# Performance work log

Hardware: AMD Instinct MI355X
Metric: run time of the kernel (lower is better)

## Reference

```python
import jax, jax.numpy as jnp
import numpy as np

B, IN_E, IN_I, D = 4096, 4096, 4096, 2048
IN_BR = 8192
BS = IN_BR // D  # block size = 4
K_E, K_I = 50, 1
E_TO_I = 50.0
BN_EPS = 1e-5


def setup_inputs() -> dict:
    key = jax.random.key(0)
    ks = jax.random.split(key, 8)
    # fan-in uniform init like nn.Linear (kaiming-uniform bound ~ 1/sqrt(in))
    def linw(k, out_f, in_f):
        b = 1.0 / np.sqrt(in_f)
        return jax.random.uniform(k, (out_f, in_f), jnp.float32, -b, b)
    return {
        "excitatory_input": jax.random.normal(ks[0], (B, IN_E), jnp.float32),
        "inhibitory_input": jax.random.normal(ks[1], (B, IN_I), jnp.float32),
        "dendrite_branch_outputs": jax.random.uniform(ks[2], (B, IN_BR), jnp.float32),
        "w_exc": linw(ks[3], D, IN_E),
        "w_inh": linw(ks[4], D, IN_I),
        "w_block": linw(ks[5], D, IN_BR),
        "bn_gamma": jnp.ones((D,), jnp.float32),
        "bn_beta": jnp.zeros((D,), jnp.float32),
    }


def _topk_linear(x, w, k):
    # keep the k largest weights per output row, zero the rest, then matmul
    idx = jax.lax.top_k(w, k)[1]                          # [D, k]
    mask = jnp.zeros_like(w).at[jnp.arange(w.shape[0])[:, None], idx].set(1.0)
    return x @ (w * mask).T                               # [B, D]


def _block_linear(x, w):
    # block-diagonal mask: row c uses columns [c*BS, (c+1)*BS)
    out_f = w.shape[0]
    wb = w.reshape(out_f, out_f, BS)[jnp.arange(out_f), jnp.arange(out_f)]  # [D, BS]
    xb = x.reshape(x.shape[0], out_f, BS)                                   # [B, D, BS]
    return jnp.einsum('bds,ds->bd', xb, wb)


def reference(excitatory_input, inhibitory_input, dendrite_branch_outputs,
              w_exc, w_inh, w_block, bn_gamma, bn_beta):
    dendrite_excitation = _topk_linear(excitatory_input, w_exc, K_E)
    dendrite_inhibition = _topk_linear(inhibitory_input, w_inh, K_I)
    dendrite_depolarization = _block_linear(dendrite_branch_outputs, w_block)
    total_excitatory = dendrite_excitation + dendrite_depolarization
    # neuron_type == 'excitatory'
    act = total_excitatory - E_TO_I * dendrite_inhibition
    # BatchNorm1d, training mode: batch stats, biased variance
    mean = jnp.mean(act, axis=0)
    var = jnp.var(act, axis=0)
    act = (act - mean) * jax.lax.rsqrt(var + BN_EPS) * bn_gamma + bn_beta
    return jax.nn.sigmoid(act)
```

## Files before the change

### kernel.cpp

```cpp
#include <hip/hip_runtime.h>
#include <hip/hip_fp16.h>

#define B_     4096
#define INE_   4096
#define INBR_  8192
#define D_     2048
#define KE_    50
#define KPAD_  52
#define CAP_   512

__device__ __forceinline__ unsigned packh2(float a, float b) {
  __half2 h = __floats2half2_rn(a, b);
  return __builtin_bit_cast(unsigned, h);
}
__device__ __forceinline__ float2 unpackh2(unsigned u) {
  __half2 h = __builtin_bit_cast(__half2, u);
  return __half22float2(h);
}

__global__ __launch_bounds__(256) void extract_diag(
    const float* __restrict__ wblock, float* __restrict__ wdiag)
{
  int d = blockIdx.x * 256 + threadIdx.x;
  float4 w = *reinterpret_cast<const float4*>(wblock + (size_t)d * (INBR_ + 4));
  reinterpret_cast<float4*>(wdiag)[d] = w;
}

__global__ __launch_bounds__(256) void topk_kernel(
    const float* __restrict__ W, int k, int kpad, float hi, float t0,
    float vscale, unsigned* __restrict__ out_off, float* __restrict__ out_val)
{
  const int row = blockIdx.x;
  const int t   = threadIdx.x;
  const float* wr = W + (size_t)row * INE_;

  __shared__ float cval[CAP_];
  __shared__ int   ccol[CAP_];
  __shared__ int   scnt;
  __shared__ int   red[4];

  float thr = t0;
  int M = 0;
  for (int attempt = 0; attempt < 8; ++attempt) {
    int local = 0;
    #pragma unroll
    for (int j = 0; j < 4; ++j) {
      float4 w4 = *reinterpret_cast<const float4*>(wr + 4 * (t + 256 * j));
      local += (w4.x > thr) + (w4.y > thr) + (w4.z > thr) + (w4.w > thr);
    }
    #pragma unroll
    for (int off = 32; off > 0; off >>= 1) local += __shfl_down(local, off);
    if ((t & 63) == 0) red[t >> 6] = local;
    __syncthreads();
    M = red[0] + red[1] + red[2] + red[3];
    __syncthreads();
    if (M >= k && M <= CAP_) break;
    if (M < k) thr = hi - (hi - thr) * 4.0f;
    else       thr = hi - (hi - thr) * 0.5f;
  }

  if (t == 0) scnt = 0;
  __syncthreads();
  #pragma unroll
  for (int j = 0; j < 4; ++j) {
    int cbase = 4 * (t + 256 * j);
    float4 w4 = *reinterpret_cast<const float4*>(wr + cbase);
    float wv[4] = {w4.x, w4.y, w4.z, w4.w};
    #pragma unroll
    for (int q = 0; q < 4; ++q) {
      if (wv[q] > thr) {
        int p = atomicAdd(&scnt, 1);
        if (p < CAP_) { cval[p] = wv[q]; ccol[p] = cbase + q; }
      }
    }
  }
  __syncthreads();
  M = scnt < CAP_ ? scnt : CAP_;

  for (int i = t; i < M; i += 256) {
    float wi = cval[i]; int ci = ccol[i];
    int rank = 0;
    for (int m = 0; m < M; ++m) {
      float wm = cval[m]; int cm = ccol[m];
      rank += (wm > wi || (wm == wi && cm < ci)) ? 1 : 0;
    }
    if (rank < k) {
      unsigned c = (unsigned)ci;
      unsigned off = ((c >> 2) << 4) | ((c & 3u) << 14);
      float    val = wi * vscale;
      if (kpad == 1) {
        out_off[row] = off;
        out_val[row] = val;
      } else {
        size_t idx = ((size_t)(rank >> 2) * D_ + row) * 4 + (rank & 3);
        out_off[idx] = off;
        out_val[idx] = val;
      }
    }
  }
  if (kpad > 1 && t < kpad - k) {
    int slot = k + t;
    size_t idx = ((size_t)(slot >> 2) * D_ + row) * 4 + (slot & 3);
    out_off[idx] = 0u;
    out_val[idx] = 0.0f;
  }
}

__device__ __forceinline__ void stage_rows(const float* __restrict__ src,
                                           unsigned* xs, int b0, int p, int Q) {
  const float* r0p = src + (size_t)(b0 + 2 * p)     * INE_;
  const float* r1p = src + (size_t)(b0 + 2 * p + 1) * INE_;
  #pragma unroll
  for (int m = 0; m < 8; ++m) {
    int c0 = 4 * Q + 512 * m;
    float4 fa = *reinterpret_cast<const float4*>(r0p + c0);
    float4 fb = *reinterpret_cast<const float4*>(r1p + c0);
    int wb = 4 * (Q + 128 * m) + p;
    xs[wb]          = packh2(fa.x, fb.x);
    xs[wb + 4096]   = packh2(fa.y, fb.y);
    xs[wb + 8192]   = packh2(fa.z, fb.z);
    xs[wb + 12288]  = packh2(fa.w, fb.w);
  }
}

#define GATH(R, OFF, WV) do {                                              \
    uint4 xq = *reinterpret_cast<const uint4*>(ldsb + (OFF));              \
    float2 f0 = unpackh2(xq.x), f1 = unpackh2(xq.y);                       \
    float2 f2 = unpackh2(xq.z), f3 = unpackh2(xq.w);                       \
    acc[R][0] = fmaf(f0.x, (WV), acc[R][0]);                               \
    acc[R][1] = fmaf(f0.y, (WV), acc[R][1]);                               \
    acc[R][2] = fmaf(f1.x, (WV), acc[R][2]);                               \
    acc[R][3] = fmaf(f1.y, (WV), acc[R][3]);                               \
    acc[R][4] = fmaf(f2.x, (WV), acc[R][4]);                               \
    acc[R][5] = fmaf(f2.y, (WV), acc[R][5]);                               \
    acc[R][6] = fmaf(f3.x, (WV), acc[R][6]);                               \
    acc[R][7] = fmaf(f3.y, (WV), acc[R][7]);                               \
  } while (0)

__global__ __launch_bounds__(512, 4) void fused_main(
    const float* __restrict__ xe, const float* __restrict__ xi,
    const float* __restrict__ xbr, const float* __restrict__ wdiag,
    const unsigned* __restrict__ soT, const float* __restrict__ veT,
    const unsigned* __restrict__ so_inh, const float* __restrict__ vi_inh,
    float* __restrict__ act)
{
  __shared__ unsigned xs[16384];
  const int t  = threadIdx.x;
  const int b0 = blockIdx.x * 8;
  const int p  = t & 3;
  const int Q  = t >> 2;

  float acc[4][8];
  #pragma unroll
  for (int r = 0; r < 4; ++r)
    #pragma unroll
    for (int b = 0; b < 8; ++b) acc[r][b] = 0.0f;

  const char* ldsb = reinterpret_cast<const char*>(xs);
  const uint4*  soT4 = reinterpret_cast<const uint4*>(soT);
  const float4* veT4 = reinterpret_cast<const float4*>(veT);

  stage_rows(xe, xs, b0, p, Q);
  __syncthreads();
  for (int ii = 0; ii < KPAD_ / 4; ++ii) {
    uint4 o[4]; float4 v[4];
    #pragma unroll
    for (int r = 0; r < 4; ++r) {
      const int d = t + 512 * r;
      o[r] = soT4[ii * D_ + d];
      v[r] = veT4[ii * D_ + d];
    }
    #pragma unroll
    for (int r = 0; r < 4; ++r) {
      GATH(r, o[r].x, v[r].x);
      GATH(r, o[r].y, v[r].y);
      GATH(r, o[r].z, v[r].z);
      GATH(r, o[r].w, v[r].w);
    }
  }
  __syncthreads();

  stage_rows(xi, xs, b0, p, Q);
  unsigned oi[4]; float vi[4];
  #pragma unroll
  for (int r = 0; r < 4; ++r) {
    const int d = t + 512 * r;
    oi[r] = so_inh[d];
    vi[r] = vi_inh[d];
  }
  __syncthreads();
  #pragma unroll
  for (int r = 0; r < 4; ++r) GATH(r, oi[r], vi[r]);

  #pragma unroll
  for (int r = 0; r < 4; ++r) {
    const int d = t + 512 * r;
    float4 wb4 = reinterpret_cast<const float4*>(wdiag)[d];
    #pragma unroll
    for (int b = 0; b < 8; ++b) {
      float4 xb4 = *reinterpret_cast<const float4*>(
          xbr + (size_t)(b0 + b) * INBR_ + 4 * d);
      acc[r][b] += xb4.x * wb4.x + xb4.y * wb4.y + xb4.z * wb4.z + xb4.w * wb4.w;
    }
  }

  #pragma unroll
  for (int r = 0; r < 4; ++r) {
    const int d = t + 512 * r;
    #pragma unroll
    for (int b = 0; b < 8; ++b)
      act[(size_t)(b0 + b) * D_ + d] = acc[r][b];
  }
}

__global__ __launch_bounds__(256) void reduce_stats(
    const float* __restrict__ act, float* __restrict__ sums,
    float* __restrict__ sumsq)
{
  const int dg = blockIdx.x & 63;
  const int rg = blockIdx.x >> 6;
  const int tx = threadIdx.x & 31;
  const int ty = threadIdx.x >> 5;
  const int d  = dg * 32 + tx;

  float s = 0.0f, s2 = 0.0f;
  #pragma unroll 4
  for (int i = 0; i < 64; ++i) {
    int row = rg * 512 + ty + 8 * i;
    float a = act[(size_t)row * D_ + d];
    s += a;
    s2 = fmaf(a, a, s2);
  }
  __shared__ float ls[2][8][32];
  ls[0][ty][tx] = s;
  ls[1][ty][tx] = s2;
  __syncthreads();
  if (ty == 0) {
    #pragma unroll
    for (int j = 1; j < 8; ++j) { s += ls[0][j][tx]; s2 += ls[1][j][tx]; }
    atomicAdd(&sums[d], s);
    atomicAdd(&sumsq[d], s2);
  }
}

__global__ __launch_bounds__(256) void finalize_stats(
    const float* __restrict__ sums, const float* __restrict__ sumsq,
    const float* __restrict__ gamma, const float* __restrict__ beta,
    float* __restrict__ scsh)
{
  int d = blockIdx.x * 256 + threadIdx.x;
  if (d < D_) {
    float mean = sums[d]  * (1.0f / B_);
    float var  = sumsq[d] * (1.0f / B_) - mean * mean;
    float rstd = rsqrtf(var + 1e-5f);
    float sc   = gamma[d] * rstd;
    scsh[2 * d]     = sc;
    scsh[2 * d + 1] = fmaf(-mean, sc, beta[d]);
  }
}

__global__ __launch_bounds__(256) void norm_sigmoid(
    float* __restrict__ act, const float* __restrict__ scsh)
{
  const int total4 = (B_ * D_) / 4;
  for (int i = blockIdx.x * blockDim.x + threadIdx.x; i < total4;
       i += gridDim.x * blockDim.x) {
    float4 a = reinterpret_cast<float4*>(act)[i];
    int d0 = (i * 4) & (D_ - 1);
    const float4* sp = reinterpret_cast<const float4*>(scsh + 2 * d0);
    float4 s0 = sp[0];
    float4 s1 = sp[1];
    float z0 = fmaf(a.x, s0.x, s0.y);
    float z1 = fmaf(a.y, s0.z, s0.w);
    float z2 = fmaf(a.z, s1.x, s1.y);
    float z3 = fmaf(a.w, s1.z, s1.w);
    a.x = 1.0f / (1.0f + __expf(-z0));
    a.y = 1.0f / (1.0f + __expf(-z1));
    a.z = 1.0f / (1.0f + __expf(-z2));
    a.w = 1.0f / (1.0f + __expf(-z3));
    reinterpret_cast<float4*>(act)[i] = a;
  }
}

extern "C" void kernel_launch(void* const* d_in, const int* in_sizes, int n_in,
                              void* d_out, int out_size, void* d_ws, size_t ws_size,
                              hipStream_t stream) {
  const float* xe    = (const float*)d_in[0];
  const float* xi    = (const float*)d_in[1];
  const float* xbr   = (const float*)d_in[2];
  const float* wexc  = (const float*)d_in[3];
  const float* winh  = (const float*)d_in[4];
  const float* wblk  = (const float*)d_in[5];
  const float* gamma = (const float*)d_in[6];
  const float* beta  = (const float*)d_in[7];
  float* act = (float*)d_out;

  char* ws = (char*)d_ws;
  unsigned* soT    = (unsigned*)(ws + 0);
  float*    veT    = (float*)   (ws + 425984);
  unsigned* so_inh = (unsigned*)(ws + 851968);
  float*    vi_inh = (float*)   (ws + 860160);
  float*    wdiag  = (float*)   (ws + 868352);
  float*    sums   = (float*)   (ws + 901120);
  float*    sumsq  = (float*)   (ws + 909312);
  float*    scsh   = (float*)   (ws + 917504);

  hipMemsetAsync(sums, 0, 2 * D_ * sizeof(float), stream);

  const float hi = 0.015625f;
  extract_diag<<<dim3(8), dim3(256), 0, stream>>>(wblk, wdiag);
  topk_kernel<<<dim3(D_), dim3(256), 0, stream>>>(
      wexc, KE_, KPAD_, hi, hi * (1.0f - 200.0f / 4096.0f), 1.0f, soT, veT);
  topk_kernel<<<dim3(D_), dim3(256), 0, stream>>>(
      winh, 1, 1, hi, hi * (1.0f - 48.0f / 4096.0f), -50.0f, so_inh, vi_inh);
  fused_main<<<dim3(B_ / 8), dim3(512), 0, stream>>>(
      xe, xi, xbr, wdiag, soT, veT, so_inh, vi_inh, act);
  reduce_stats<<<dim3(512), dim3(256), 0, stream>>>(act, sums, sumsq);
  finalize_stats<<<dim3((D_ + 255) / 256), dim3(256), 0, stream>>>(
      sums, sumsq, gamma, beta, scsh);
  norm_sigmoid<<<dim3(2048), dim3(256), 0, stream>>>(act, scsh);
}
```

Baseline: 140.0 us.

## Merge prep kernels, split branch term out of main, fuse BN finalize into sigmoid

The top-k selections for both weight matrices and the diagonal extraction now run in a single prep launch. The block-diagonal branch term moves out of the gather kernel into a separate elementwise kernel that reads and rewrites act. The gather loop is restructured to issue LDS loads in batches before the FMAs. The finalize step is folded into the norm/sigmoid kernel, with each block recomputing scale and shift into shared memory. The aim is fewer launches and better latency hiding in the gather, at the cost of an extra full read-modify-write pass over act and redundant per-block statistics computation.

```diff
diff --git a/kernel.cpp b/kernel.cpp
--- a/kernel.cpp
+++ b/kernel.cpp
@@ -18,20 +18,11 @@
   return __half22float2(h);
 }
 
-__global__ __launch_bounds__(256) void extract_diag(
-    const float* __restrict__ wblock, float* __restrict__ wdiag)
-{
-  int d = blockIdx.x * 256 + threadIdx.x;
-  float4 w = *reinterpret_cast<const float4*>(wblock + (size_t)d * (INBR_ + 4));
-  reinterpret_cast<float4*>(wdiag)[d] = w;
-}
-
-__global__ __launch_bounds__(256) void topk_kernel(
-    const float* __restrict__ W, int k, int kpad, float hi, float t0,
-    float vscale, unsigned* __restrict__ out_off, float* __restrict__ out_val)
-{
-  const int row = blockIdx.x;
-  const int t   = threadIdx.x;
+__device__ void topk_body(const float* __restrict__ W, int row, int k, int kpad,
+                          float hi, float t0, float vscale,
+                          unsigned* __restrict__ out_off, float* __restrict__ out_val)
+{
+  const int t = threadIdx.x;
   const float* wr = W + (size_t)row * INE_;
 
   __shared__ float cval[CAP_];
@@ -69,8 +60,8 @@
     #pragma unroll
     for (int q = 0; q < 4; ++q) {
       if (wv[q] > thr) {
-        int p = atomicAdd(&scnt, 1);
-        if (p < CAP_) { cval[p] = wv[q]; ccol[p] = cbase + q; }
+        int pp = atomicAdd(&scnt, 1);
+        if (pp < CAP_) { cval[pp] = wv[q]; ccol[pp] = cbase + q; }
       }
     }
   }
@@ -106,8 +97,34 @@
   }
 }
 
-__device__ __forceinline__ void stage_rows(const float* __restrict__ src,
-                                           unsigned* xs, int b0, int p, int Q) {
+__global__ __launch_bounds__(256) void prep_kernel(
+    const float* __restrict__ wexc, const float* __restrict__ winh,
+    const float* __restrict__ wblk,
+    unsigned* __restrict__ soT, float* __restrict__ veT,
+    unsigned* __restrict__ so_inh, float* __restrict__ vi_inh,
+    float* __restrict__ wdiag)
+{
+  const int bid = blockIdx.x;
+  const float hi = 0.015625f;
+  if (bid < 2048) {
+    topk_body(wexc, bid, KE_, KPAD_, hi, hi * (1.0f - 200.0f / 4096.0f), 1.0f,
+              soT, veT);
+  } else if (bid < 4096) {
+    topk_body(winh, bid - 2048, 1, 1, hi, hi * (1.0f - 48.0f / 4096.0f), -50.0f,
+              so_inh, vi_inh);
+  } else {
+    const int t = threadIdx.x;
+    #pragma unroll
+    for (int j = 0; j < 8; ++j) {
+      int d = t + 256 * j;
+      float4 w = *reinterpret_cast<const float4*>(wblk + (size_t)d * (INBR_ + 4));
+      reinterpret_cast<float4*>(wdiag)[d] = w;
+    }
+  }
+}
+
+__device__ __forceinline__ void stage_rows8(const float* __restrict__ src,
+                                            unsigned* xs, int b0, int p, int Q) {
   const float* r0p = src + (size_t)(b0 + 2 * p)     * INE_;
   const float* r1p = src + (size_t)(b0 + 2 * p + 1) * INE_;
   #pragma unroll
@@ -123,10 +140,13 @@
   }
 }
 
-#define GATH(R, OFF, WV) do {                                              \
-    uint4 xq = *reinterpret_cast<const uint4*>(ldsb + (OFF));              \
-    float2 f0 = unpackh2(xq.x), f1 = unpackh2(xq.y);                       \
-    float2 f2 = unpackh2(xq.z), f3 = unpackh2(xq.w);                       \
+__device__ __forceinline__ uint4 ld16(const char* ldsb, unsigned off) {
+  return *reinterpret_cast<const uint4*>(ldsb + off);
+}
+
+#define FMA8(R, G, WV) do {                                                \
+    float2 f0 = unpackh2((G).x), f1 = unpackh2((G).y);                     \
+    float2 f2 = unpackh2((G).z), f3 = unpackh2((G).w);                     \
     acc[R][0] = fmaf(f0.x, (WV), acc[R][0]);                               \
     acc[R][1] = fmaf(f0.y, (WV), acc[R][1]);                               \
     acc[R][2] = fmaf(f1.x, (WV), acc[R][2]);                               \
@@ -137,9 +157,8 @@
     acc[R][7] = fmaf(f3.y, (WV), acc[R][7]);                               \
   } while (0)
 
-__global__ __launch_bounds__(512, 4) void fused_main(
+__global__ __launch_bounds__(512, 4) void ei_kernel(
     const float* __restrict__ xe, const float* __restrict__ xi,
-    const float* __restrict__ xbr, const float* __restrict__ wdiag,
     const unsigned* __restrict__ soT, const float* __restrict__ veT,
     const unsigned* __restrict__ so_inh, const float* __restrict__ vi_inh,
     float* __restrict__ act)
@@ -160,56 +179,99 @@
   const uint4*  soT4 = reinterpret_cast<const uint4*>(soT);
   const float4* veT4 = reinterpret_cast<const float4*>(veT);
 
-  stage_rows(xe, xs, b0, p, Q);
+  stage_rows8(xe, xs, b0, p, Q);
   __syncthreads();
   for (int ii = 0; ii < KPAD_ / 4; ++ii) {
     uint4 o[4]; float4 v[4];
     #pragma unroll
     for (int r = 0; r < 4; ++r) {
-      const int d = t + 512 * r;
-      o[r] = soT4[ii * D_ + d];
-      v[r] = veT4[ii * D_ + d];
-    }
-    #pragma unroll
-    for (int r = 0; r < 4; ++r) {
-      GATH(r, o[r].x, v[r].x);
-      GATH(r, o[r].y, v[r].y);
-      GATH(r, o[r].z, v[r].z);
-      GATH(r, o[r].w, v[r].w);
-    }
-  }
-  __syncthreads();
-
-  stage_rows(xi, xs, b0, p, Q);
-  unsigned oi[4]; float vi[4];
+      o[r] = soT4[ii * D_ + t + 512 * r];
+      v[r] = veT4[ii * D_ + t + 512 * r];
+    }
+    {
+      uint4 g[2][4];
+      #pragma unroll
+      for (int rr = 0; rr < 2; ++rr) {
+        g[rr][0] = ld16(ldsb, o[rr].x);
+        g[rr][1] = ld16(ldsb, o[rr].y);
+        g[rr][2] = ld16(ldsb, o[rr].z);
+        g[rr][3] = ld16(ldsb, o[rr].w);
+      }
+      #pragma unroll
+      for (int rr = 0; rr < 2; ++rr) {
+        FMA8(rr, g[rr][0], v[rr].x);
+        FMA8(rr, g[rr][1], v[rr].y);
+        FMA8(rr, g[rr][2], v[rr].z);
+        FMA8(rr, g[rr][3], v[rr].w);
+      }
+    }
+    {
+      uint4 g[2][4];
+      #pragma unroll
+      for (int rr = 0; rr < 2; ++rr) {
+        g[rr][0] = ld16(ldsb, o[2 + rr].x);
+        g[rr][1] = ld16(ldsb, o[2 + rr].y);
+        g[rr][2] = ld16(ldsb, o[2 + rr].z);
+        g[rr][3] = ld16(ldsb, o[2 + rr].w);
+      }
+      #pragma unroll
+      for (int rr = 0; rr < 2; ++rr) {
+        FMA8(2 + rr, g[rr][0], v[2 + rr].x);
+        FMA8(2 + rr, g[rr][1], v[2 + rr].y);
+        FMA8(2 + rr, g[rr][2], v[2 + rr].z);
+        FMA8(2 + rr, g[rr][3], v[2 + rr].w);
+      }
+    }
+  }
+  __syncthreads();
+
+  stage_rows8(xi, xs, b0, p, Q);
+  unsigned oi[4]; float viv[4];
+  #pragma unroll
+  for (int r = 0; r < 4; ++r) {
+    oi[r]  = so_inh[t + 512 * r];
+    viv[r] = vi_inh[t + 512 * r];
+  }
+  __syncthreads();
+  {
+    uint4 gi[4];
+    #pragma unroll
+    for (int r = 0; r < 4; ++r) gi[r] = ld16(ldsb, oi[r]);
+    #pragma unroll
+    for (int r = 0; r < 4; ++r) FMA8(r, gi[r], viv[r]);
+  }
+
   #pragma unroll
   for (int r = 0; r < 4; ++r) {
     const int d = t + 512 * r;
-    oi[r] = so_inh[d];
-    vi[r] = vi_inh[d];
-  }
-  __syncthreads();
-  #pragma unroll
-  for (int r = 0; r < 4; ++r) GATH(r, oi[r], vi[r]);
-
-  #pragma unroll
-  for (int r = 0; r < 4; ++r) {
-    const int d = t + 512 * r;
-    float4 wb4 = reinterpret_cast<const float4*>(wdiag)[d];
-    #pragma unroll
-    for (int b = 0; b < 8; ++b) {
-      float4 xb4 = *reinterpret_cast<const float4*>(
-          xbr + (size_t)(b0 + b) * INBR_ + 4 * d);
-      acc[r][b] += xb4.x * wb4.x + xb4.y * wb4.y + xb4.z * wb4.z + xb4.w * wb4.w;
-    }
-  }
-
-  #pragma unroll
-  for (int r = 0; r < 4; ++r) {
-    const int d = t + 512 * r;
     #pragma unroll
     for (int b = 0; b < 8; ++b)
       act[(size_t)(b0 + b) * D_ + d] = acc[r][b];
+  }
+}
+
+__global__ __launch_bounds__(256) void br_kernel(
+    const float* __restrict__ xbr, const float* __restrict__ wdiag,
+    float* __restrict__ act)
+{
+  const float4* xbr4 = reinterpret_cast<const float4*>(xbr);
+  const float4* wd4  = reinterpret_cast<const float4*>(wdiag);
+  float4*       act4 = reinterpret_cast<float4*>(act);
+  const int total = B_ * D_ / 4;
+  for (int i = blockIdx.x * 256 + threadIdx.x; i < total;
+       i += gridDim.x * 256) {
+    int b  = i >> 9;
+    int dq = i & 511;
+    float4 a = act4[i];
+    const float4* xp = xbr4 + (size_t)b * (INBR_ / 4) + 4 * dq;
+    float4 x0 = xp[0], x1 = xp[1], x2 = xp[2], x3 = xp[3];
+    float4 w0 = wd4[4 * dq], w1 = wd4[4 * dq + 1],
+           w2 = wd4[4 * dq + 2], w3 = wd4[4 * dq + 3];
+    a.x += x0.x * w0.x + x0.y * w0.y + x0.z * w0.z + x0.w * w0.w;
+    a.y += x1.x * w1.x + x1.y * w1.y + x1.z * w1.z + x1.w * w1.w;
+    a.z += x2.x * w2.x + x2.y * w2.y + x2.z * w2.z + x2.w * w2.w;
+    a.w += x3.x * w3.x + x3.y * w3.y + x3.z * w3.z + x3.w * w3.w;
+    act4[i] = a;
   }
 }
 
@@ -243,13 +305,16 @@
   }
 }
 
-__global__ __launch_bounds__(256) void finalize_stats(
-    const float* __restrict__ sums, const float* __restrict__ sumsq,
-    const float* __restrict__ gamma, const float* __restrict__ beta,
-    float* __restrict__ scsh)
-{
-  int d = blockIdx.x * 256 + threadIdx.x;
-  if (d < D_) {
+__global__ __launch_bounds__(256) void tail_kernel(
+    float* __restrict__ act, const float* __restrict__ sums,
+    const float* __restrict__ sumsq, const float* __restrict__ gamma,
+    const float* __restrict__ beta)
+{
+  __shared__ float scsh[2 * D_];
+  const int tid = threadIdx.x;
+  #pragma unroll
+  for (int j = 0; j < 8; ++j) {
+    int d = tid + 256 * j;
     float mean = sums[d]  * (1.0f / B_);
     float var  = sumsq[d] * (1.0f / B_) - mean * mean;
     float rstd = rsqrtf(var + 1e-5f);
@@ -257,28 +322,28 @@
     scsh[2 * d]     = sc;
     scsh[2 * d + 1] = fmaf(-mean, sc, beta[d]);
   }
-}
-
-__global__ __launch_bounds__(256) void norm_sigmoid(
-    float* __restrict__ act, const float* __restrict__ scsh)
-{
-  const int total4 = (B_ * D_) / 4;
-  for (int i = blockIdx.x * blockDim.x + threadIdx.x; i < total4;
-       i += gridDim.x * blockDim.x) {
-    float4 a = reinterpret_cast<float4*>(act)[i];
-    int d0 = (i * 4) & (D_ - 1);
-    const float4* sp = reinterpret_cast<const float4*>(scsh + 2 * d0);
-    float4 s0 = sp[0];
-    float4 s1 = sp[1];
-    float z0 = fmaf(a.x, s0.x, s0.y);
-    float z1 = fmaf(a.y, s0.z, s0.w);
-    float z2 = fmaf(a.z, s1.x, s1.y);
-    float z3 = fmaf(a.w, s1.z, s1.w);
-    a.x = 1.0f / (1.0f + __expf(-z0));
-    a.y = 1.0f / (1.0f + __expf(-z1));
-    a.z = 1.0f / (1.0f + __expf(-z2));
-    a.w = 1.0f / (1.0f + __expf(-z3));
-    reinterpret_cast<float4*>(act)[i] = a;
+  __syncthreads();
+
+  const int r0 = blockIdx.x * 8;
+  for (int rr = 0; rr < 8; ++rr) {
+    float4* rowp = reinterpret_cast<float4*>(act + (size_t)(r0 + rr) * D_);
+    #pragma unroll
+    for (int i2 = 0; i2 < 2; ++i2) {
+      int i = tid + 256 * i2;
+      float4 a = rowp[i];
+      const float4* sp = reinterpret_cast<const float4*>(scsh + 8 * i);
+      float4 s0 = sp[0];
+      float4 s1 = sp[1];
+      float z0 = fmaf(a.x, s0.x, s0.y);
+      float z1 = fmaf(a.y, s0.z, s0.w);
+      float z2 = fmaf(a.z, s1.x, s1.y);
+      float z3 = fmaf(a.w, s1.z, s1.w);
+      a.x = 1.0f / (1.0f + __expf(-z0));
+      a.y = 1.0f / (1.0f + __expf(-z1));
+      a.z = 1.0f / (1.0f + __expf(-z2));
+      a.w = 1.0f / (1.0f + __expf(-z3));
+      rowp[i] = a;
+    }
   }
 }
 
@@ -303,20 +368,15 @@
   float*    wdiag  = (float*)   (ws + 868352);
   float*    sums   = (float*)   (ws + 901120);
   float*    sumsq  = (float*)   (ws + 909312);
-  float*    scsh   = (float*)   (ws + 917504);
 
   hipMemsetAsync(sums, 0, 2 * D_ * sizeof(float), stream);
 
-  const float hi = 0.015625f;
-  extract_diag<<<dim3(8), dim3(256), 0, stream>>>(wblk, wdiag);
-  topk_kernel<<<dim3(D_), dim3(256), 0, stream>>>(
-      wexc, KE_, KPAD_, hi, hi * (1.0f - 200.0f / 4096.0f), 1.0f, soT, veT);
-  topk_kernel<<<dim3(D_), dim3(256), 0, stream>>>(
-      winh, 1, 1, hi, hi * (1.0f - 48.0f / 4096.0f), -50.0f, so_inh, vi_inh);
-  fused_main<<<dim3(B_ / 8), dim3(512), 0, stream>>>(
-      xe, xi, xbr, wdiag, soT, veT, so_inh, vi_inh, act);
+  prep_kernel<<<dim3(4097), dim3(256), 0, stream>>>(
+      wexc, winh, wblk, soT, veT, so_inh, vi_inh, wdiag);
+  ei_kernel<<<dim3(B_ / 8), dim3(512), 0, stream>>>(
+      xe, xi, soT, veT, so_inh, vi_inh, act);
+  br_kernel<<<dim3(2048), dim3(256), 0, stream>>>(xbr, wdiag, act);
   reduce_stats<<<dim3(512), dim3(256), 0, stream>>>(act, sums, sumsq);
-  finalize_stats<<<dim3((D_ + 255) / 256), dim3(256), 0, stream>>>(
-      sums, sumsq, gamma, beta, scsh);
-  norm_sigmoid<<<dim3(2048), dim3(256), 0, stream>>>(act, scsh);
-}
+  tail_kernel<<<dim3(512), dim3(256), 0, stream>>>(
+      act, sums, sumsq, gamma, beta);
+}
```

Result: faster. 135.7 us (-3.1%).
